# Kernel tuning notes

Hardware: AMD Instinct MI355X
Metric: run time of the kernel (lower is better)

Reference implementation:

```python
import jax, jax.numpy as jnp
import numpy as np

N, E, G = 40000, 640000, 64
DIN, DH, H, DE = 64, 64, 2, 16
HD = H * DH  # 128
NEG_SLOPE_GAT = 0.2
NEG_SLOPE_ACT = 0.01
EPS_BN = 1e-5


def _p(k, shape, fan_in):
    return jax.random.normal(k, shape, dtype=jnp.float32) * (1.0 / np.sqrt(fan_in))


def setup_inputs() -> dict:
    key = jax.random.key(0)
    ks = jax.random.split(key, 32)
    inp = {
        'x': jax.random.normal(ks[0], (N, DIN), dtype=jnp.float32),
        'edge_index': jax.random.randint(ks[1], (2, E), 0, N, dtype=jnp.int32),
        'edge_attr': jax.random.normal(ks[2], (E, DE), dtype=jnp.float32),
        'batch': jnp.sort(jax.random.randint(ks[3], (N,), 0, G, dtype=jnp.int32)),
    }
    dims_in = [DIN, HD, HD]
    k = 4
    for i in (1, 2, 3):
        din = dims_in[i - 1]
        inp[f'w{i}l'] = _p(ks[k], (din, HD), din); k += 1
        inp[f'w{i}r'] = _p(ks[k], (din, HD), din); k += 1
        inp[f'w{i}e'] = _p(ks[k], (DE, HD), DE); k += 1
        inp[f'a{i}'] = _p(ks[k], (H, DH), DH); k += 1
        inp[f'cb{i}'] = jnp.zeros((HD,), dtype=jnp.float32)
        inp[f'g{i}'] = jnp.ones((HD,), dtype=jnp.float32)
        inp[f'bb{i}'] = jnp.zeros((HD,), dtype=jnp.float32)
    inp['fc1w'] = _p(ks[k], (HD, DH), HD); k += 1
    inp['fc1b'] = jnp.zeros((DH,), dtype=jnp.float32)
    inp['fc2w'] = _p(ks[k], (DH, 1), DH); k += 1
    inp['fc2b'] = jnp.zeros((1,), dtype=jnp.float32)
    return inp


def _gatv2(x, src, dst, ea, wl, wr, we, att, bias):
    # x:[N,din], src/dst:[Ef] (self-loops included), ea:[Ef,DE]
    xl = (x @ wl).reshape(-1, H, DH)            # source transform [N,H,C]
    xr = (x @ wr).reshape(-1, H, DH)            # target transform
    ee = (ea @ we).reshape(-1, H, DH)           # edge transform [Ef,H,C]
    m = xl[src] + xr[dst] + ee                  # GATv2 pre-activation [Ef,H,C]
    s = jnp.einsum('ehc,hc->eh', jax.nn.leaky_relu(m, NEG_SLOPE_GAT), att)
    smax = jax.ops.segment_max(s, dst, num_segments=N)
    ex = jnp.exp(s - smax[dst])
    den = jax.ops.segment_sum(ex, dst, num_segments=N)
    alpha = ex / (den[dst] + 1e-16)             # segment softmax over in-edges
    out = jax.ops.segment_sum(alpha[:, :, None] * xl[src], dst, num_segments=N)
    return out.reshape(-1, HD) + bias


def _bn(x, g, b):
    mu = jnp.mean(x, axis=0)
    var = jnp.mean((x - mu) ** 2, axis=0)
    return (x - mu) * jax.lax.rsqrt(var + EPS_BN) * g + b


def reference(x, edge_index, edge_attr, batch,
              w1l, w1r, w1e, a1, cb1, g1, bb1,
              w2l, w2r, w2e, a2, cb2, g2, bb2,
              w3l, w3r, w3e, a3, cb3, g3, bb3,
              fc1w, fc1b, fc2w, fc2b):
    src, dst = edge_index[0], edge_index[1]
    # add self-loops with fill_value='mean' edge attrs (mean over incoming edges)
    deg = jax.ops.segment_sum(jnp.ones((E,), jnp.float32), dst, num_segments=N)
    loop_attr = jax.ops.segment_sum(edge_attr, dst, num_segments=N) / jnp.clip(deg, 1.0)[:, None]
    ar = jnp.arange(N, dtype=src.dtype)
    src_f = jnp.concatenate([src, ar])
    dst_f = jnp.concatenate([dst, ar])
    ea_f = jnp.concatenate([edge_attr, loop_attr], axis=0)

    h = jax.nn.leaky_relu(_bn(_gatv2(x, src_f, dst_f, ea_f, w1l, w1r, w1e, a1, cb1), g1, bb1), NEG_SLOPE_ACT)
    h = jax.nn.leaky_relu(_bn(_gatv2(h, src_f, dst_f, ea_f, w2l, w2r, w2e, a2, cb2), g2, bb2), NEG_SLOPE_ACT)
    h = jax.nn.leaky_relu(_bn(_gatv2(h, src_f, dst_f, ea_f, w3l, w3r, w3e, a3, cb3), g3, bb3), NEG_SLOPE_ACT)

    # global mean pool over graphs
    cnt = jax.ops.segment_sum(jnp.ones((N,), jnp.float32), batch, num_segments=G)
    pooled = jax.ops.segment_sum(h, batch, num_segments=G) / jnp.clip(cnt, 1.0)[:, None]

    hh = jax.nn.relu(pooled @ fc1w + fc1b)  # dropout is identity at inference
    return hh @ fc2w + fc2b
```

## Files before the change

kernel.cpp:

```cpp
#include <hip/hip_runtime.h>
#include <hip/hip_fp16.h>
#include <math.h>

#define NN 40000
#define NE 640000
#define NG 64
#define DINV 64
#define HDV 128
#define DEV 16
#define EF (NE + NN)
#define PSPLIT 16
#define NSB ((NN + 255) / 256)

typedef float v2f __attribute__((ext_vector_type(2)));

__device__ __forceinline__ int chan_of_pos(int p) { return (p >> 1) + 64 * (p & 1); }

template <int CTRL>
__device__ __forceinline__ float dpp_mov_f(float x) {
    return __builtin_bit_cast(float,
        __builtin_amdgcn_update_dpp(0, __builtin_bit_cast(int, x), CTRL, 0xf, 0xf, true));
}
__device__ __forceinline__ float wave_sum64(float x) {
    x += dpp_mov_f<0x111>(x);
    x += dpp_mov_f<0x112>(x);
    x += dpp_mov_f<0x114>(x);
    x += dpp_mov_f<0x118>(x);
    x += dpp_mov_f<0x142>(x);
    x += dpp_mov_f<0x143>(x);
    return __builtin_bit_cast(float, __builtin_amdgcn_readlane(__builtin_bit_cast(int, x), 63));
}


__global__ void k_count(const int* __restrict__ dst, int* __restrict__ cnt) {
    int e = blockIdx.x * 256 + threadIdx.x;
    if (e < NE) atomicAdd(&cnt[dst[e]], 1);
}

__global__ __launch_bounds__(256) void k_scan_a(const int* __restrict__ cnt, int* __restrict__ bsum) {
    int i = blockIdx.x * 256 + threadIdx.x;
    int v = (i < NN) ? cnt[i] + 1 : 0;
    __shared__ int s[256];
    s[threadIdx.x] = v;
    __syncthreads();
    for (int off = 128; off > 0; off >>= 1) {
        if (threadIdx.x < off) s[threadIdx.x] += s[threadIdx.x + off];
        __syncthreads();
    }
    if (threadIdx.x == 0) bsum[blockIdx.x] = s[0];
}

__global__ __launch_bounds__(256) void k_scan_b(const int* __restrict__ bsum, int* __restrict__ boff) {
    int t = threadIdx.x;
    int v = (t < NSB) ? bsum[t] : 0;
    __shared__ int s[256];
    s[t] = v;
    __syncthreads();
    for (int off = 1; off < 256; off <<= 1) {
        int add = (t >= off) ? s[t - off] : 0;
        __syncthreads();
        s[t] += add;
        __syncthreads();
    }
    boff[t] = s[t] - v;
}

__global__ __launch_bounds__(256) void k_scan_c(const int* __restrict__ cnt, const int* __restrict__ boff,
                                                int* __restrict__ rowptr, int* __restrict__ cursor) {
    int i = blockIdx.x * 256 + threadIdx.x;
    int t = threadIdx.x;
    int v = (i < NN) ? cnt[i] + 1 : 0;
    __shared__ int s[256];
    s[t] = v;
    __syncthreads();
    for (int off = 1; off < 256; off <<= 1) {
        int add = (t >= off) ? s[t - off] : 0;
        __syncthreads();
        s[t] += add;
        __syncthreads();
    }
    int excl = boff[blockIdx.x] + s[t] - v;
    if (i < NN) {
        rowptr[i] = excl;
        cursor[i] = excl;
        if (i == NN - 1) rowptr[NN] = excl + v;
    }
}

__global__ void k_fill(const int* __restrict__ src, const int* __restrict__ dst,
                       const float* __restrict__ edge_attr,
                       int* __restrict__ cursor, int* __restrict__ csr_src, float* __restrict__ csr_ea) {
    int e = blockIdx.x * 256 + threadIdx.x;
    if (e < NE) {
        int d = dst[e];
        int p = atomicAdd(&cursor[d], 1);
        csr_src[p] = src[e];
        const float4* s4 = (const float4*)&edge_attr[(size_t)e * DEV];
        float4* d4 = (float4*)&csr_ea[(size_t)p * DEV];
        d4[0] = s4[0]; d4[1] = s4[1]; d4[2] = s4[2]; d4[3] = s4[3];
    }
}

__global__ void k_wperm_all(const float* __restrict__ w1l, const float* __restrict__ w1r,
                            const float* __restrict__ w2l, const float* __restrict__ w2r,
                            const float* __restrict__ w3l, const float* __restrict__ w3r,
                            float* __restrict__ wlp, float* __restrict__ wrp,
                            const int* __restrict__ batch, int* __restrict__ gstart) {
    int t = threadIdx.x;
    if (blockIdx.x == gridDim.x - 1) {
        int g = t;
        if (g > NG) return;
        int lo = 0, hi = NN;
        while (lo < hi) {
            int mid = (lo + hi) >> 1;
            if (batch[mid] < g) lo = mid + 1; else hi = mid;
        }
        gstart[g] = lo;
        return;
    }
    int i = blockIdx.x * 256 + t;
    if (i >= 3 * HDV * HDV) return;
    int layer = i / (HDV * HDV);
    int r = i - layer * HDV * HDV;
    int p = r & 127, kp = r >> 7;
    int K = (layer == 0) ? DINV : HDV;
    if (kp >= K) return;
    int kr = (layer == 0) ? kp : chan_of_pos(kp);
    int cc = chan_of_pos(p);
    const float* wl = (layer == 0) ? w1l : (layer == 1) ? w2l : w3l;
    const float* wr = (layer == 0) ? w1r : (layer == 1) ? w2r : w3r;
    wlp[i] = wl[kr * HDV + cc];
    wrp[i] = wr[kr * HDV + cc];
}

__global__ __launch_bounds__(256) void k_gemm(const float* __restrict__ A, int K,
                                              const float* __restrict__ Wl, const float* __restrict__ Wr,
                                              __half* __restrict__ XLh, float* __restrict__ XR,
                                              const double* __restrict__ bnsum, const double* __restrict__ bnsumsq,
                                              const float* __restrict__ g, const float* __restrict__ bb) {
    __shared__ float As[2][8][128];
    __shared__ float Bs[2][8][128];
    __shared__ float ssc[HDV], ssh[HDV];
    int t = threadIdx.x;
    if (bnsum && t < HDV) {
        int c = chan_of_pos(t);
        double mu = bnsum[t] * (1.0 / NN);
        double var = bnsumsq[t] * (1.0 / NN) - mu * mu;
        double inv = rsqrt(var + 1e-5);
        float sc = (float)(inv * (double)g[c]);
        ssc[t] = sc;
        ssh[t] = bb[c] - (float)mu * sc;
    }
    __syncthreads();
    int rb = blockIdx.x * 128;
    const float* __restrict__ Bg = blockIdx.y ? Wr : Wl;
    int tx = t & 15, ty = t >> 4;
    int lr_ = t >> 1, lk = (t & 1) * 4;
    int bk = t >> 5, bc = (t & 31) * 4;

    auto loadA = [&](int k0) -> float4 {
        float4 av = (rb + lr_ < NN) ? *(const float4*)&A[(size_t)(rb + lr_) * K + k0 + lk]
                                    : float4{0.f, 0.f, 0.f, 0.f};
        if (bnsum) {
            int c0 = k0 + lk;
            av.x = fmaf(av.x, ssc[c0 + 0], ssh[c0 + 0]); av.x = fmaxf(av.x, 0.01f * av.x);
            av.y = fmaf(av.y, ssc[c0 + 1], ssh[c0 + 1]); av.y = fmaxf(av.y, 0.01f * av.y);
            av.z = fmaf(av.z, ssc[c0 + 2], ssh[c0 + 2]); av.z = fmaxf(av.z, 0.01f * av.z);
            av.w = fmaf(av.w, ssc[c0 + 3], ssh[c0 + 3]); av.w = fmaxf(av.w, 0.01f * av.w);
        }
        return av;
    };

    float4 av = loadA(0);
    float4 bv = *(const float4*)&Bg[(size_t)bk * HDV + bc];
    As[0][lk + 0][lr_] = av.x; As[0][lk + 1][lr_] = av.y; As[0][lk + 2][lr_] = av.z; As[0][lk + 3][lr_] = av.w;
    *(float4*)&Bs[0][bk][bc] = bv;
    __syncthreads();

    float acc[8][8] = {};
    int cur = 0;
    for (int k0 = 0; k0 < K; k0 += 8) {
        bool more = (k0 + 8) < K;
        if (more) {
            av = loadA(k0 + 8);
            bv = *(const float4*)&Bg[(size_t)(k0 + 8 + bk) * HDV + bc];
        }
        #pragma unroll
        for (int kk = 0; kk < 8; ++kk) {
            float a8[8], b8[8];
            *(float4*)&a8[0] = *(const float4*)&As[cur][kk][ty * 8];
            *(float4*)&a8[4] = *(const float4*)&As[cur][kk][ty * 8 + 4];
            *(float4*)&b8[0] = *(const float4*)&Bs[cur][kk][tx * 8];
            *(float4*)&b8[4] = *(const float4*)&Bs[cur][kk][tx * 8 + 4];
            #pragma unroll
            for (int ii = 0; ii < 8; ++ii)
                #pragma unroll
                for (int jj = 0; jj < 8; ++jj)
                    acc[ii][jj] = fmaf(a8[ii], b8[jj], acc[ii][jj]);
        }
        if (more) {
            int nxt = cur ^ 1;
            As[nxt][lk + 0][lr_] = av.x; As[nxt][lk + 1][lr_] = av.y;
            As[nxt][lk + 2][lr_] = av.z; As[nxt][lk + 3][lr_] = av.w;
            *(float4*)&Bs[nxt][bk][bc] = bv;
            __syncthreads();
            cur = nxt;
        }
    }
    if (blockIdx.y == 0) {
        #pragma unroll
        for (int ii = 0; ii < 8; ++ii) {
            int row = rb + ty * 8 + ii;
            if (row < NN) {
                __half2 h4[4];
                #pragma unroll
                for (int jj = 0; jj < 4; ++jj)
                    h4[jj] = __half2{__float2half_rn(acc[ii][2 * jj]), __float2half_rn(acc[ii][2 * jj + 1])};
                *(__half2*)&XLh[(size_t)row * HDV + tx * 8 + 0] = h4[0];
                *(__half2*)&XLh[(size_t)row * HDV + tx * 8 + 2] = h4[1];
                *(__half2*)&XLh[(size_t)row * HDV + tx * 8 + 4] = h4[2];
                *(__half2*)&XLh[(size_t)row * HDV + tx * 8 + 6] = h4[3];
            }
        }
    } else {
        #pragma unroll
        for (int ii = 0; ii < 8; ++ii) {
            int row = rb + ty * 8 + ii;
            if (row < NN) {
                float4 v0 = {acc[ii][0], acc[ii][1], acc[ii][2], acc[ii][3]};
                float4 v1 = {acc[ii][4], acc[ii][5], acc[ii][6], acc[ii][7]};
                *(float4*)&XR[(size_t)row * HDV + tx * 8] = v0;
                *(float4*)&XR[(size_t)row * HDV + tx * 8 + 4] = v1;
            }
        }
    }
}

__global__ __launch_bounds__(256) void k_gat(const __half* __restrict__ XLh, const float* __restrict__ XR,
                                             const int* __restrict__ rowptr, const int* __restrict__ csr_src,
                                             const float* __restrict__ csr_ea,
                                             const float* __restrict__ we, const float* __restrict__ att,
                                             const float* __restrict__ cb, float* __restrict__ hpre) {
    int t = threadIdx.x;
    int L = t & 63;
    int d = __builtin_amdgcn_readfirstlane(blockIdx.x * 4 + (t >> 6));
    v2f rwe0[DEV / 2], rwe1[DEV / 2];
    #pragma unroll
    for (int j = 0; j < DEV / 2; ++j) {
        rwe0[j] = v2f{we[(2 * j) * HDV + L],      we[(2 * j + 1) * HDV + L]};
        rwe1[j] = v2f{we[(2 * j) * HDV + 64 + L], we[(2 * j + 1) * HDV + 64 + L]};
    }
    const float LOG2E = 1.4426950408889634f;
    float attv0 = att[L] * LOG2E, attv1 = att[64 + L] * LOG2E;
    v2f xr = *(const v2f*)&XR[(size_t)d * HDV + 2 * L];
    int istart = rowptr[d];
    int iend = rowptr[d + 1] - 1;
    int deg = iend - istart;
    v2f Da = {0.f, 0.f}, Db = {0.f, 0.f}, Aa = {0.f, 0.f}, Ab = {0.f, 0.f};
    v2f eesum = {0.f, 0.f};

    auto body = [&](int i, v2f& Dk, v2f& Ak) {
        int sx = csr_src[i];
        const v2f* eap = (const v2f*)(csr_ea + (size_t)i * DEV);
        unsigned off = ((unsigned)sx << 8) + ((unsigned)L << 2);
        __half2 xlh = *(const __half2*)((const char*)XLh + off);
        v2f xl = {__half2float(xlh.x), __half2float(xlh.y)};
        v2f e0 = {0.f, 0.f}, e1 = {0.f, 0.f};
        #pragma unroll
        for (int j = 0; j < DEV / 2; ++j) {
            v2f ea2 = eap[j];
            e0 = __builtin_elementwise_fma(ea2, rwe0[j], e0);
            e1 = __builtin_elementwise_fma(ea2, rwe1[j], e1);
        }
        v2f eev = {e0.x + e0.y, e1.x + e1.y};
        eesum += eev;
        v2f m = xl + xr + eev;
        v2f lr = __builtin_elementwise_max(m, m * 0.2f);
        float c0 = wave_sum64(lr.x * attv0);
        float c1 = wave_sum64(lr.y * attv1);
        v2f e = {__builtin_amdgcn_exp2f(c0), __builtin_amdgcn_exp2f(c1)};
        Dk += e;
        Ak = __builtin_elementwise_fma(e, xl, Ak);
    };

    int i = istart;
    if (deg & 1) { body(i, Da, Aa); ++i; }
    for (; i < iend; i += 2) {
        body(i,     Da, Aa);
        body(i + 1, Db, Ab);
    }
    {
        __half2 xlh = *(const __half2*)&XLh[(size_t)d * HDV + 2 * L];
        v2f xls = {__half2float(xlh.x), __half2float(xlh.y)};
        v2f eeself = eesum * (1.0f / (float)max(deg, 1));
        v2f m = xls + xr + eeself;
        v2f lr = __builtin_elementwise_max(m, m * 0.2f);
        float c0 = wave_sum64(lr.x * attv0);
        float c1 = wave_sum64(lr.y * attv1);
        v2f e = {__builtin_amdgcn_exp2f(c0), __builtin_amdgcn_exp2f(c1)};
        Da += e;
        Aa = __builtin_elementwise_fma(e, xls, Aa);
    }
    v2f D = Da + Db;
    v2f A = Aa + Ab;
    v2f h = A / (D + 1e-16f) + v2f{cb[L], cb[64 + L]};
    *(v2f*)&hpre[(size_t)d * HDV + 2 * L] = h;
}


__global__ __launch_bounds__(256) void k_bn_stats(const float* __restrict__ hpre,
                                                  double* __restrict__ bnsum, double* __restrict__ bnsumsq) {
    int c2 = (threadIdx.x & 63) * 2;
    int rg = threadIdx.x >> 6;
    int r0 = blockIdx.x * 250;
    v2f s = {0.f, 0.f}, q = {0.f, 0.f};
    for (int r = r0 + rg; r < r0 + 250; r += 4) {
        v2f v = *(const v2f*)&hpre[(size_t)r * HDV + c2];
        s += v;
        q = __builtin_elementwise_fma(v, v, q);
    }
    __shared__ v2f ls[256], lq[256];
    ls[threadIdx.x] = s; lq[threadIdx.x] = q;
    __syncthreads();
    if (rg == 0) {
        int b = threadIdx.x;
        s = ls[b] + ls[b + 64] + ls[b + 128] + ls[b + 192];
        q = lq[b] + lq[b + 64] + lq[b + 128] + lq[b + 192];
        atomicAdd(&bnsum[c2],     (double)s.x);
        atomicAdd(&bnsum[c2 + 1], (double)s.y);
        atomicAdd(&bnsumsq[c2],     (double)q.x);
        atomicAdd(&bnsumsq[c2 + 1], (double)q.y);
    }
}


__global__ __launch_bounds__(256) void k_pool2(const float* __restrict__ hpre, const int* __restrict__ gstart,
                                               const double* __restrict__ bnsum, const double* __restrict__ bnsumsq,
                                               const float* __restrict__ g, const float* __restrict__ bb,
                                               float* __restrict__ pooled_sum) {
    __shared__ float ssc[HDV], ssh[HDV];
    int t = threadIdx.x;
    if (t < HDV) {
        int cc = chan_of_pos(t);
        double mu = bnsum[t] * (1.0 / NN);
        double var = bnsumsq[t] * (1.0 / NN) - mu * mu;
        double inv = rsqrt(var + 1e-5);
        float sc = (float)(inv * (double)g[cc]);
        ssc[t] = sc;
        ssh[t] = bb[cc] - (float)mu * sc;
    }
    __syncthreads();
    int gr = blockIdx.x, slice = blockIdx.y;
    int s = gstart[gr], e = gstart[gr + 1];
    int c = t & 127, half = t >> 7;
    float sc = ssc[c], sh = ssh[c];
    float acc = 0.f;
    for (int r = s + slice * 2 + half; r < e; r += PSPLIT * 2) {
        float v = fmaf(hpre[(size_t)r * HDV + c], sc, sh);
        acc += fmaxf(v, 0.01f * v);
    }
    __shared__ float ls[256];
    ls[t] = acc;
    __syncthreads();
    if (half == 0) atomicAdd(&pooled_sum[gr * HDV + c], acc + ls[t + 128]);
}

__global__ __launch_bounds__(512) void k_mlp(const float* __restrict__ pooled_sum, const int* __restrict__ gstart,
                                             const float* __restrict__ fc1w, const float* __restrict__ fc1b,
                                             const float* __restrict__ fc2w, const float* __restrict__ fc2b,
                                             float* __restrict__ out) {
    __shared__ float pl[NG * HDV];
    __shared__ float hh[NG * 64];
    int t = threadIdx.x;
    for (int i = t; i < NG * HDV; i += 512) {
        int gr = i >> 7;
        float cnt = (float)max(gstart[gr + 1] - gstart[gr], 1);
        pl[i] = pooled_sum[i] / cnt;
    }
    __syncthreads();
    for (int i = t; i < NG * 64; i += 512) {
        int gr = i >> 6, c = i & 63;
        float s = fc1b[c];
        for (int p = 0; p < HDV; ++p)
            s += pl[gr * HDV + p] * fc1w[chan_of_pos(p) * 64 + c];
        hh[i] = s > 0.f ? s : 0.f;
    }
    __syncthreads();
    if (t < NG) {
        float s = fc2b[0];
        for (int k = 0; k < 64; ++k) s += hh[t * 64 + k] * fc2w[k];
        out[t] = s;
    }
}


extern "C" void kernel_launch(void* const* d_in, const int* in_sizes, int n_in,
                              void* d_out, int out_size, void* d_ws, size_t ws_size,
                              hipStream_t stream) {
    const float* x = (const float*)d_in[0];
    const int* ei = (const int*)d_in[1];
    const int* src = ei;
    const int* dst = ei + NE;
    const float* ea = (const float*)d_in[2];
    const int* batch = (const int*)d_in[3];
    const float* fc1w = (const float*)d_in[25];
    const float* fc1b = (const float*)d_in[26];
    const float* fc2w = (const float*)d_in[27];
    const float* fc2b = (const float*)d_in[28];
    float* out = (float*)d_out;

    char* ws = (char*)d_ws;
    size_t off = 0;
    auto alloc = [&](size_t bytes) -> void* {
        void* p = ws + off;
        off = (off + bytes + 255) & ~(size_t)255;
        return p;
    };

    int* cnt = (int*)alloc(NN * 4);
    double* bnsum = (double*)alloc(3 * HDV * 8);
    double* bnsumsq = (double*)alloc(3 * HDV * 8);
    float* pooled_sum = (float*)alloc(NG * HDV * 4);
    size_t zero_bytes = off;

    int* rowptr = (int*)alloc((NN + 1) * 4);
    int* cursor = (int*)alloc(NN * 4);
    int* gstart = (int*)alloc((NG + 1) * 4);
    int* bsum = (int*)alloc(NSB * 4);
    int* boff = (int*)alloc(256 * 4);
    float* wlp = (float*)alloc(3 * HDV * HDV * 4);
    float* wrp = (float*)alloc(3 * HDV * HDV * 4);
    int* csr_src = (int*)alloc(((size_t)EF + 16) * 4);
    float* csr_ea = (float*)alloc(((size_t)EF * DEV + 64) * 4);
    __half* XLh = (__half*)alloc((size_t)NN * HDV * 2);
    float* XRb = (float*)alloc((size_t)NN * HDV * 4);
    float* hpre = (float*)alloc((size_t)NN * HDV * 4);
    (void)ws_size; (void)in_sizes; (void)n_in; (void)out_size;

    hipMemsetAsync(d_ws, 0, zero_bytes, stream);

    k_count<<<(NE + 255) / 256, 256, 0, stream>>>(dst, cnt);
    k_scan_a<<<NSB, 256, 0, stream>>>(cnt, bsum);
    k_scan_b<<<1, 256, 0, stream>>>(bsum, boff);
    k_scan_c<<<NSB, 256, 0, stream>>>(cnt, boff, rowptr, cursor);
    k_fill<<<(NE + 255) / 256, 256, 0, stream>>>(src, dst, ea, cursor, csr_src, csr_ea);
    k_wperm_all<<<(3 * HDV * HDV + 255) / 256 + 1, 256, 0, stream>>>(
        (const float*)d_in[4], (const float*)d_in[5],
        (const float*)d_in[11], (const float*)d_in[12],
        (const float*)d_in[18], (const float*)d_in[19], wlp, wrp, batch, gstart);

    const float* actp = x;
    int K = DINV;
    for (int L = 0; L < 3; ++L) {
        const float* we = (const float*)d_in[4 + 7 * L + 2];
        const float* a  = (const float*)d_in[4 + 7 * L + 3];
        const float* cb = (const float*)d_in[4 + 7 * L + 4];

        const double* bs  = (L == 0) ? nullptr : bnsum + (size_t)(L - 1) * HDV;
        const double* bsq = (L == 0) ? nullptr : bnsumsq + (size_t)(L - 1) * HDV;
        const float* gg   = (L == 0) ? nullptr : (const float*)d_in[4 + 7 * (L - 1) + 5];
        const float* bbp  = (L == 0) ? nullptr : (const float*)d_in[4 + 7 * (L - 1) + 6];

        k_gemm<<<dim3((NN + 127) / 128, 2), 256, 0, stream>>>(
            actp, K, wlp + (size_t)L * HDV * HDV, wrp + (size_t)L * HDV * HDV,
            XLh, XRb, bs, bsq, gg, bbp);
        k_gat<<<NN / 4, 256, 0, stream>>>(XLh, XRb, rowptr, csr_src, csr_ea, we, a, cb, hpre);
        k_bn_stats<<<160, 256, 0, stream>>>(hpre, bnsum + (size_t)L * HDV, bnsumsq + (size_t)L * HDV);
        actp = hpre;
        K = HDV;
    }

    k_pool2<<<dim3(NG, PSPLIT), 256, 0, stream>>>(
        hpre, gstart, bnsum + 2 * HDV, bnsumsq + 2 * HDV,
        (const float*)d_in[4 + 7 * 2 + 5], (const float*)d_in[4 + 7 * 2 + 6], pooled_sum);
    k_mlp<<<1, 512, 0, stream>>>(pooled_sum, gstart, fc1w, fc1b, fc2w, fc2b, out);
}
```

Measured before the change: 520.8 us.

## Assign each half-wave one attention head to halve cross-lane reductions

```diff
diff --git a/kernel.cpp b/kernel.cpp
--- a/kernel.cpp
+++ b/kernel.cpp
@@ -14,21 +14,22 @@
 
 typedef float v2f __attribute__((ext_vector_type(2)));
 
-__device__ __forceinline__ int chan_of_pos(int p) { return (p >> 1) + 64 * (p & 1); }
+__device__ __forceinline__ int chan_of_pos(int p) { return ((p >> 2) << 1) + (p & 1) + (((p >> 1) & 1) << 6); }
 
 template <int CTRL>
 __device__ __forceinline__ float dpp_mov_f(float x) {
     return __builtin_bit_cast(float,
         __builtin_amdgcn_update_dpp(0, __builtin_bit_cast(int, x), CTRL, 0xf, 0xf, true));
 }
-__device__ __forceinline__ float wave_sum64(float x) {
+__device__ __forceinline__ v2f half_sums(float x) {
     x += dpp_mov_f<0x111>(x);
     x += dpp_mov_f<0x112>(x);
     x += dpp_mov_f<0x114>(x);
     x += dpp_mov_f<0x118>(x);
     x += dpp_mov_f<0x142>(x);
-    x += dpp_mov_f<0x143>(x);
-    return __builtin_bit_cast(float, __builtin_amdgcn_readlane(__builtin_bit_cast(int, x), 63));
+    float s0 = __builtin_bit_cast(float, __builtin_amdgcn_readlane(__builtin_bit_cast(int, x), 31));
+    float s1 = __builtin_bit_cast(float, __builtin_amdgcn_readlane(__builtin_bit_cast(int, x), 63));
+    return v2f{s0, s1};
 }
 
 
@@ -243,26 +244,31 @@
                                              const float* __restrict__ cb, float* __restrict__ hpre) {
     int t = threadIdx.x;
     int L = t & 63;
+    int l5 = L & 31, hh = L >> 5;
+    int c0 = hh * 64 + 2 * l5;
+    int poff = 4 * l5 + 2 * hh;
     int d = __builtin_amdgcn_readfirstlane(blockIdx.x * 4 + (t >> 6));
     v2f rwe0[DEV / 2], rwe1[DEV / 2];
     #pragma unroll
     for (int j = 0; j < DEV / 2; ++j) {
-        rwe0[j] = v2f{we[(2 * j) * HDV + L],      we[(2 * j + 1) * HDV + L]};
-        rwe1[j] = v2f{we[(2 * j) * HDV + 64 + L], we[(2 * j + 1) * HDV + 64 + L]};
+        rwe0[j] = v2f{we[(2 * j) * HDV + c0],     we[(2 * j + 1) * HDV + c0]};
+        rwe1[j] = v2f{we[(2 * j) * HDV + c0 + 1], we[(2 * j + 1) * HDV + c0 + 1]};
     }
     const float LOG2E = 1.4426950408889634f;
-    float attv0 = att[L] * LOG2E, attv1 = att[64 + L] * LOG2E;
-    v2f xr = *(const v2f*)&XR[(size_t)d * HDV + 2 * L];
+    v2f attv = {att[c0] * LOG2E, att[c0 + 1] * LOG2E};
+    v2f xr = *(const v2f*)&XR[(size_t)d * HDV + poff];
     int istart = rowptr[d];
     int iend = rowptr[d + 1] - 1;
     int deg = iend - istart;
-    v2f Da = {0.f, 0.f}, Db = {0.f, 0.f}, Aa = {0.f, 0.f}, Ab = {0.f, 0.f};
+    float Da = 0.f, Db = 0.f;
+    v2f Aa = {0.f, 0.f}, Ab = {0.f, 0.f};
     v2f eesum = {0.f, 0.f};
-
-    auto body = [&](int i, v2f& Dk, v2f& Ak) {
+    unsigned xoff = ((unsigned)poff << 1);
+
+    auto body = [&](int i, float& Dk, v2f& Ak) {
         int sx = csr_src[i];
         const v2f* eap = (const v2f*)(csr_ea + (size_t)i * DEV);
-        unsigned off = ((unsigned)sx << 8) + ((unsigned)L << 2);
+        unsigned off = ((unsigned)sx << 8) + xoff;
         __half2 xlh = *(const __half2*)((const char*)XLh + off);
         v2f xl = {__half2float(xlh.x), __half2float(xlh.y)};
         v2f e0 = {0.f, 0.f}, e1 = {0.f, 0.f};
@@ -276,11 +282,13 @@
         eesum += eev;
         v2f m = xl + xr + eev;
         v2f lr = __builtin_elementwise_max(m, m * 0.2f);
-        float c0 = wave_sum64(lr.x * attv0);
-        float c1 = wave_sum64(lr.y * attv1);
-        v2f e = {__builtin_amdgcn_exp2f(c0), __builtin_amdgcn_exp2f(c1)};
-        Dk += e;
-        Ak = __builtin_elementwise_fma(e, xl, Ak);
+        float cl = fmaf(lr.y, attv.y, lr.x * attv.x);
+        v2f s = half_sums(cl);
+        float es0 = __builtin_amdgcn_exp2f(s.x);
+        float es1 = __builtin_amdgcn_exp2f(s.y);
+        float es = hh ? es1 : es0;
+        Dk += es;
+        Ak = __builtin_elementwise_fma(v2f{es, es}, xl, Ak);
     };
 
     int i = istart;
@@ -290,21 +298,24 @@
         body(i + 1, Db, Ab);
     }
     {
-        __half2 xlh = *(const __half2*)&XLh[(size_t)d * HDV + 2 * L];
+        __half2 xlh = *(const __half2*)&XLh[(size_t)d * HDV + poff];
         v2f xls = {__half2float(xlh.x), __half2float(xlh.y)};
         v2f eeself = eesum * (1.0f / (float)max(deg, 1));
         v2f m = xls + xr + eeself;
         v2f lr = __builtin_elementwise_max(m, m * 0.2f);
-        float c0 = wave_sum64(lr.x * attv0);
-        float c1 = wave_sum64(lr.y * attv1);
-        v2f e = {__builtin_amdgcn_exp2f(c0), __builtin_amdgcn_exp2f(c1)};
-        Da += e;
-        Aa = __builtin_elementwise_fma(e, xls, Aa);
-    }
-    v2f D = Da + Db;
+        float cl = fmaf(lr.y, attv.y, lr.x * attv.x);
+        v2f s = half_sums(cl);
+        float es0 = __builtin_amdgcn_exp2f(s.x);
+        float es1 = __builtin_amdgcn_exp2f(s.y);
+        float es = hh ? es1 : es0;
+        Da += es;
+        Aa = __builtin_elementwise_fma(v2f{es, es}, xls, Aa);
+    }
+    float D = Da + Db;
     v2f A = Aa + Ab;
-    v2f h = A / (D + 1e-16f) + v2f{cb[L], cb[64 + L]};
-    *(v2f*)&hpre[(size_t)d * HDV + 2 * L] = h;
+    float dinv = 1.0f / (D + 1e-16f);
+    v2f h = A * v2f{dinv, dinv} + v2f{cb[c0], cb[c0 + 1]};
+    *(v2f*)&hpre[(size_t)d * HDV + poff] = h;
 }
 
 
```

After: 494.8 us. 5.0% less time.
